# Optimization experiments

Measured on AMD Instinct MI355X. Metric: run time of the kernel, lower is better.

## Reference

```python
import jax, jax.numpy as jnp
import numpy as np

DELTA = 0.1      # delta from __init__
LN_EPS = 1e-5    # torch LayerNorm default eps

B, IN, OUT, E = 256, 512, 512, 256


def setup_inputs() -> dict:
    key = jax.random.key(0)
    ks = jax.random.split(key, 6)
    return {
        "x": jax.random.normal(ks[0], (B, IN), dtype=jnp.float32),
        # nn.init.normal_(std=0.1), shape (out_features, in_features)
        "weights": 0.1 * jax.random.normal(ks[1], (OUT, IN), dtype=jnp.float32),
        # frozen predicate embeddings (in_features, embedding_dim)
        "pred_emb": jax.random.normal(ks[2], (IN, E), dtype=jnp.float32),
        # nn.Linear(E, OUT): weight (OUT, E), bias (OUT,)
        "attn_w": jax.random.uniform(ks[3], (OUT, E), dtype=jnp.float32,
                                      minval=-1.0, maxval=1.0) / np.sqrt(E),
        "attn_b": jax.random.uniform(ks[4], (OUT,), dtype=jnp.float32,
                                      minval=-1.0, maxval=1.0) / np.sqrt(E),
        # nn.LayerNorm(OUT)
        "ln_g": jnp.ones((OUT,), dtype=jnp.float32),
        "ln_b": jnp.zeros((OUT,), dtype=jnp.float32),
    }


def _layernorm(s, g, b):
    mu = s.mean(axis=-1, keepdims=True)
    var = ((s - mu) ** 2).mean(axis=-1, keepdims=True)
    return (s - mu) * jax.lax.rsqrt(var + LN_EPS) * g + b


def reference(x, weights, pred_emb, attn_w, attn_b, ln_g, ln_b):
    # semantic attention gate: batch-invariant, compute once -> (IN, OUT)
    scores = pred_emb @ attn_w.T + attn_b                    # (IN, OUT)
    sig = jax.nn.sigmoid(_layernorm(scores, ln_g, ln_b))     # (IN, OUT)

    xe = x[:, :, None]                                       # (B, IN, 1)
    wt = weights.T[None]                                     # (1, IN, OUT)
    # abs_weight * attn_adjusted, fused elementwise -> (B, IN, OUT)
    aw = jnp.abs(xe * wt) * (sig[None] * xe)

    bias = aw.max(axis=1) - aw.sum(axis=1)                   # CONJUNCTION: max - sum
    return x @ weights.T + DELTA * bias                      # (B, OUT)
```

## Files before the change

### kernel.cpp

```cpp
#include <hip/hip_runtime.h>
#include <hip/hip_bf16.h>
#include <math.h>

#define B_   256
#define IN_  512
#define OUT_ 512
#define E_   256
#define DELTA_ 0.1f
#define LN_EPS_ 1e-5f

__global__ __launch_bounds__(512)
void k1_scores_ln_sig(const float* __restrict__ pred_emb,
                      const float* __restrict__ attn_w,
                      const float* __restrict__ attn_b,
                      const float* __restrict__ ln_g,
                      const float* __restrict__ ln_b,
                      const float* __restrict__ weights,
                      float2* __restrict__ wv) {
    __shared__ float pe[2][E_];
    __shared__ float red[8][2][2];
    __shared__ float smu[2], srs[2];

    const int t    = threadIdx.x;
    const int lane = t & 63;
    const int wid  = t >> 6;
    const int i0   = blockIdx.x * 2;
    const int o    = t;

    pe[t >> 8][t & 255] = pred_emb[(size_t)(i0 + (t >> 8)) * E_ + (t & 255)];
    __syncthreads();

    const float4* p0 = reinterpret_cast<const float4*>(pe[0]);
    const float4* p1 = reinterpret_cast<const float4*>(pe[1]);
    const float4* wrow = reinterpret_cast<const float4*>(attn_w + (size_t)o * E_);

    float a0 = 0.f, a1 = 0.f;
    #pragma unroll 8
    for (int e4 = 0; e4 < E_ / 4; ++e4) {
        float4 w4 = wrow[e4];
        float4 q0 = p0[e4];
        float4 q1 = p1[e4];
        a0 += q0.x * w4.x + q0.y * w4.y + q0.z * w4.z + q0.w * w4.w;
        a1 += q1.x * w4.x + q1.y * w4.y + q1.z * w4.z + q1.w * w4.w;
    }
    const float bo = attn_b[o];
    a0 += bo;
    a1 += bo;

    {
        float s1 = a0, s2 = a0 * a0;
        float u1 = a1, u2 = a1 * a1;
        #pragma unroll
        for (int off = 32; off > 0; off >>= 1) {
            s1 += __shfl_down(s1, off);
            s2 += __shfl_down(s2, off);
            u1 += __shfl_down(u1, off);
            u2 += __shfl_down(u2, off);
        }
        if (lane == 0) {
            red[wid][0][0] = s1; red[wid][0][1] = s2;
            red[wid][1][0] = u1; red[wid][1][1] = u2;
        }
    }
    __syncthreads();
    if (t < 2) {
        float s1 = 0.f, s2 = 0.f;
        #pragma unroll
        for (int w = 0; w < 8; ++w) { s1 += red[w][t][0]; s2 += red[w][t][1]; }
        float mu  = s1 / (float)OUT_;
        float var = s2 / (float)OUT_ - mu * mu;
        smu[t] = mu;
        srs[t] = rsqrtf(var + LN_EPS_);
    }
    __syncthreads();

    const float g  = ln_g[o];
    const float bb = ln_b[o];
    float z0 = (a0 - smu[0]) * srs[0] * g + bb;
    float z1 = (a1 - smu[1]) * srs[1] * g + bb;
    float sg0 = 1.f / (1.f + expf(-z0));
    float sg1 = 1.f / (1.f + expf(-z1));

    float2 w01 = *reinterpret_cast<const float2*>(weights + (size_t)o * IN_ + i0);
    wv[(size_t)(i0 + 0) * OUT_ + o] = make_float2(w01.x, fabsf(w01.x) * sg0);
    wv[(size_t)(i0 + 1) * OUT_ + o] = make_float2(w01.y, fabsf(w01.y) * sg1);
}

#define K2_SK 4
#define K2_CH 128
#define K2_BO (B_ * OUT_)

__global__ __launch_bounds__(256)
void k2_partials(const float* __restrict__ x,
                 const float2* __restrict__ wv,
                 float* __restrict__ plin,
                 float* __restrict__ pmax) {
    __shared__ float4 xs4[64 * 33];
    __shared__ float2 ws2[K2_CH * 17];

    const int t  = threadIdx.x;
    const int ot = t & 15;
    const int bl = t >> 4;
    const int o0 = blockIdx.x * 16;
    const int b0 = blockIdx.y * 64;
    const int sk = blockIdx.z;
    const int i0 = sk * K2_CH;

    #pragma unroll
    for (int k = 0; k < 8; ++k) {
        int p    = t + k * 256;
        int row  = p >> 5;
        int col4 = p & 31;
        xs4[row * 33 + col4] = reinterpret_cast<const float4*>(
            x + (size_t)(b0 + row) * IN_ + i0)[col4];
    }
    #pragma unroll
    for (int k = 0; k < 8; ++k) {
        int r = bl + 16 * k;
        ws2[r * 17 + ot] = wv[(size_t)(i0 + r) * OUT_ + o0 + ot];
    }
    __syncthreads();

    const int o = o0 + ot;
    float d0 = 0.f, s0 = 0.f, m0 = -INFINITY;
    float d1 = 0.f, s1 = 0.f, m1 = -INFINITY;
    float d2 = 0.f, s2 = 0.f, m2 = -INFINITY;
    float d3 = 0.f, s3 = 0.f, m3 = -INFINITY;

    #pragma unroll 2
    for (int i4 = 0; i4 < K2_CH / 4; ++i4) {
        float4 x0 = xs4[(bl +  0) * 33 + i4];
        float4 x1 = xs4[(bl + 16) * 33 + i4];
        float4 x2 = xs4[(bl + 32) * 33 + i4];
        float4 x3 = xs4[(bl + 48) * 33 + i4];
        float2 w0 = ws2[(4 * i4 + 0) * 17 + ot];
        float2 w1 = ws2[(4 * i4 + 1) * 17 + ot];
        float2 w2 = ws2[(4 * i4 + 2) * 17 + ot];
        float2 w3 = ws2[(4 * i4 + 3) * 17 + ot];
        float p;
        float4 u0 = make_float4(x0.x * fabsf(x0.x), x0.y * fabsf(x0.y),
                                x0.z * fabsf(x0.z), x0.w * fabsf(x0.w));
        float4 u1 = make_float4(x1.x * fabsf(x1.x), x1.y * fabsf(x1.y),
                                x1.z * fabsf(x1.z), x1.w * fabsf(x1.w));
        float4 u2 = make_float4(x2.x * fabsf(x2.x), x2.y * fabsf(x2.y),
                                x2.z * fabsf(x2.z), x2.w * fabsf(x2.w));
        float4 u3 = make_float4(x3.x * fabsf(x3.x), x3.y * fabsf(x3.y),
                                x3.z * fabsf(x3.z), x3.w * fabsf(x3.w));

        d0 = fmaf(x0.x, w0.x, d0); p = u0.x * w0.y; s0 += p; m0 = fmaxf(m0, p);
        d1 = fmaf(x1.x, w0.x, d1); p = u1.x * w0.y; s1 += p; m1 = fmaxf(m1, p);
        d2 = fmaf(x2.x, w0.x, d2); p = u2.x * w0.y; s2 += p; m2 = fmaxf(m2, p);
        d3 = fmaf(x3.x, w0.x, d3); p = u3.x * w0.y; s3 += p; m3 = fmaxf(m3, p);

        d0 = fmaf(x0.y, w1.x, d0); p = u0.y * w1.y; s0 += p; m0 = fmaxf(m0, p);
        d1 = fmaf(x1.y, w1.x, d1); p = u1.y * w1.y; s1 += p; m1 = fmaxf(m1, p);
        d2 = fmaf(x2.y, w1.x, d2); p = u2.y * w1.y; s2 += p; m2 = fmaxf(m2, p);
        d3 = fmaf(x3.y, w1.x, d3); p = u3.y * w1.y; s3 += p; m3 = fmaxf(m3, p);

        d0 = fmaf(x0.z, w2.x, d0); p = u0.z * w2.y; s0 += p; m0 = fmaxf(m0, p);
        d1 = fmaf(x1.z, w2.x, d1); p = u1.z * w2.y; s1 += p; m1 = fmaxf(m1, p);
        d2 = fmaf(x2.z, w2.x, d2); p = u2.z * w2.y; s2 += p; m2 = fmaxf(m2, p);
        d3 = fmaf(x3.z, w2.x, d3); p = u3.z * w2.y; s3 += p; m3 = fmaxf(m3, p);

        d0 = fmaf(x0.w, w3.x, d0); p = u0.w * w3.y; s0 += p; m0 = fmaxf(m0, p);
        d1 = fmaf(x1.w, w3.x, d1); p = u1.w * w3.y; s1 += p; m1 = fmaxf(m1, p);
        d2 = fmaf(x2.w, w3.x, d2); p = u2.w * w3.y; s2 += p; m2 = fmaxf(m2, p);
        d3 = fmaf(x3.w, w3.x, d3); p = u3.w * w3.y; s3 += p; m3 = fmaxf(m3, p);
    }

    const size_t base = (size_t)sk * K2_BO + (size_t)b0 * OUT_ + o;
    plin[base + (size_t)(bl +  0) * OUT_] = d0 - DELTA_ * s0;
    plin[base + (size_t)(bl + 16) * OUT_] = d1 - DELTA_ * s1;
    plin[base + (size_t)(bl + 32) * OUT_] = d2 - DELTA_ * s2;
    plin[base + (size_t)(bl + 48) * OUT_] = d3 - DELTA_ * s3;
    pmax[base + (size_t)(bl +  0) * OUT_] = m0;
    pmax[base + (size_t)(bl + 16) * OUT_] = m1;
    pmax[base + (size_t)(bl + 32) * OUT_] = m2;
    pmax[base + (size_t)(bl + 48) * OUT_] = m3;
}

__global__ __launch_bounds__(256)
void k3_combine(const float4* __restrict__ plin4,
                const float4* __restrict__ pmax4,
                float4* __restrict__ out4) {
    const int g = blockIdx.x * 256 + threadIdx.x;
    const int Q = K2_BO / 4;
    float4 l0 = plin4[g], l1 = plin4[Q + g], l2 = plin4[2 * Q + g], l3 = plin4[3 * Q + g];
    float4 m0 = pmax4[g], m1 = pmax4[Q + g], m2 = pmax4[2 * Q + g], m3 = pmax4[3 * Q + g];
    float4 r;
    r.x = (l0.x + l1.x + l2.x + l3.x) + DELTA_ * fmaxf(fmaxf(m0.x, m1.x), fmaxf(m2.x, m3.x));
    r.y = (l0.y + l1.y + l2.y + l3.y) + DELTA_ * fmaxf(fmaxf(m0.y, m1.y), fmaxf(m2.y, m3.y));
    r.z = (l0.z + l1.z + l2.z + l3.z) + DELTA_ * fmaxf(fmaxf(m0.z, m1.z), fmaxf(m2.z, m3.z));
    r.w = (l0.w + l1.w + l2.w + l3.w) + DELTA_ * fmaxf(fmaxf(m0.w, m1.w), fmaxf(m2.w, m3.w));
    out4[g] = r;
}

extern "C" void kernel_launch(void* const* d_in, const int* in_sizes, int n_in,
                              void* d_out, int out_size, void* d_ws, size_t ws_size,
                              hipStream_t stream) {
    const float* x        = (const float*)d_in[0];
    const float* weights  = (const float*)d_in[1];
    const float* pred_emb = (const float*)d_in[2];
    const float* attn_w   = (const float*)d_in[3];
    const float* attn_b   = (const float*)d_in[4];
    const float* ln_g     = (const float*)d_in[5];
    const float* ln_b     = (const float*)d_in[6];

    float2* wv   = (float2*)d_ws;
    float*  plin = (float*)d_ws + 2 * (size_t)IN_ * OUT_;
    float*  pmax = plin + (size_t)K2_SK * K2_BO;

    k1_scores_ln_sig<<<IN_ / 2, 512, 0, stream>>>(
        pred_emb, attn_w, attn_b, ln_g, ln_b, weights, wv);

    k2_partials<<<dim3(OUT_ / 16, B_ / 64, K2_SK), 256, 0, stream>>>(
        x, wv, plin, pmax);

    k3_combine<<<K2_BO / 4 / 256, 256, 0, stream>>>(
        (const float4*)plin, (const float4*)pmax, (float4*)d_out);
}
```

Measured before the change: 99.59 us.

## Remove split-K partials and combine kernel; loop over full IN in one kernel

```diff
diff --git a/kernel.cpp b/kernel.cpp
--- a/kernel.cpp
+++ b/kernel.cpp
@@ -86,113 +86,73 @@
     wv[(size_t)(i0 + 1) * OUT_ + o] = make_float2(w01.y, fabsf(w01.y) * sg1);
 }
 
-#define K2_SK 4
 #define K2_CH 128
-#define K2_BO (B_ * OUT_)
 
 __global__ __launch_bounds__(256)
-void k2_partials(const float* __restrict__ x,
-                 const float2* __restrict__ wv,
-                 float* __restrict__ plin,
-                 float* __restrict__ pmax) {
-    __shared__ float4 xs4[64 * 33];
+void k2_full(const float* __restrict__ x,
+             const float2* __restrict__ wv,
+             float* __restrict__ out) {
+    __shared__ float4 xs4[32 * 33];
     __shared__ float2 ws2[K2_CH * 17];
 
     const int t  = threadIdx.x;
     const int ot = t & 15;
     const int bl = t >> 4;
     const int o0 = blockIdx.x * 16;
-    const int b0 = blockIdx.y * 64;
-    const int sk = blockIdx.z;
-    const int i0 = sk * K2_CH;
+    const int b0 = blockIdx.y * 32;
+    const int o  = o0 + ot;
 
-    #pragma unroll
-    for (int k = 0; k < 8; ++k) {
-        int p    = t + k * 256;
-        int row  = p >> 5;
-        int col4 = p & 31;
-        xs4[row * 33 + col4] = reinterpret_cast<const float4*>(
-            x + (size_t)(b0 + row) * IN_ + i0)[col4];
-    }
-    #pragma unroll
-    for (int k = 0; k < 8; ++k) {
-        int r = bl + 16 * k;
-        ws2[r * 17 + ot] = wv[(size_t)(i0 + r) * OUT_ + o0 + ot];
-    }
-    __syncthreads();
-
-    const int o = o0 + ot;
     float d0 = 0.f, s0 = 0.f, m0 = -INFINITY;
     float d1 = 0.f, s1 = 0.f, m1 = -INFINITY;
-    float d2 = 0.f, s2 = 0.f, m2 = -INFINITY;
-    float d3 = 0.f, s3 = 0.f, m3 = -INFINITY;
 
-    #pragma unroll 2
-    for (int i4 = 0; i4 < K2_CH / 4; ++i4) {
-        float4 x0 = xs4[(bl +  0) * 33 + i4];
-        float4 x1 = xs4[(bl + 16) * 33 + i4];
-        float4 x2 = xs4[(bl + 32) * 33 + i4];
-        float4 x3 = xs4[(bl + 48) * 33 + i4];
-        float2 w0 = ws2[(4 * i4 + 0) * 17 + ot];
-        float2 w1 = ws2[(4 * i4 + 1) * 17 + ot];
-        float2 w2 = ws2[(4 * i4 + 2) * 17 + ot];
-        float2 w3 = ws2[(4 * i4 + 3) * 17 + ot];
-        float p;
-        float4 u0 = make_float4(x0.x * fabsf(x0.x), x0.y * fabsf(x0.y),
-                                x0.z * fabsf(x0.z), x0.w * fabsf(x0.w));
-        float4 u1 = make_float4(x1.x * fabsf(x1.x), x1.y * fabsf(x1.y),
-                                x1.z * fabsf(x1.z), x1.w * fabsf(x1.w));
-        float4 u2 = make_float4(x2.x * fabsf(x2.x), x2.y * fabsf(x2.y),
-                                x2.z * fabsf(x2.z), x2.w * fabsf(x2.w));
-        float4 u3 = make_float4(x3.x * fabsf(x3.x), x3.y * fabsf(x3.y),
-                                x3.z * fabsf(x3.z), x3.w * fabsf(x3.w));
+    for (int c = 0; c < IN_ / K2_CH; ++c) {
+        if (c) __syncthreads();
+        const int i0 = c * K2_CH;
 
-        d0 = fmaf(x0.x, w0.x, d0); p = u0.x * w0.y; s0 += p; m0 = fmaxf(m0, p);
-        d1 = fmaf(x1.x, w0.x, d1); p = u1.x * w0.y; s1 += p; m1 = fmaxf(m1, p);
-        d2 = fmaf(x2.x, w0.x, d2); p = u2.x * w0.y; s2 += p; m2 = fmaxf(m2, p);
-        d3 = fmaf(x3.x, w0.x, d3); p = u3.x * w0.y; s3 += p; m3 = fmaxf(m3, p);
+        #pragma unroll
+        for (int k = 0; k < 4; ++k) {
+            int p    = t + k * 256;
+            int row  = p >> 5;
+            int col4 = p & 31;
+            xs4[row * 33 + col4] = reinterpret_cast<const float4*>(
+                x + (size_t)(b0 + row) * IN_ + i0)[col4];
+        }
+        #pragma unroll
+        for (int k = 0; k < 8; ++k) {
+            int r = bl + 16 * k;
+            ws2[r * 17 + ot] = wv[(size_t)(i0 + r) * OUT_ + o0 + ot];
+        }
+        __syncthreads();
 
-        d0 = fmaf(x0.y, w1.x, d0); p = u0.y * w1.y; s0 += p; m0 = fmaxf(m0, p);
-        d1 = fmaf(x1.y, w1.x, d1); p = u1.y * w1.y; s1 += p; m1 = fmaxf(m1, p);
-        d2 = fmaf(x2.y, w1.x, d2); p = u2.y * w1.y; s2 += p; m2 = fmaxf(m2, p);
-        d3 = fmaf(x3.y, w1.x, d3); p = u3.y * w1.y; s3 += p; m3 = fmaxf(m3, p);
-
-        d0 = fmaf(x0.z, w2.x, d0); p = u0.z * w2.y; s0 += p; m0 = fmaxf(m0, p);
-        d1 = fmaf(x1.z, w2.x, d1); p = u1.z * w2.y; s1 += p; m1 = fmaxf(m1, p);
-        d2 = fmaf(x2.z, w2.x, d2); p = u2.z * w2.y; s2 += p; m2 = fmaxf(m2, p);
-        d3 = fmaf(x3.z, w2.x, d3); p = u3.z * w2.y; s3 += p; m3 = fmaxf(m3, p);
-
-        d0 = fmaf(x0.w, w3.x, d0); p = u0.w * w3.y; s0 += p; m0 = fmaxf(m0, p);
-        d1 = fmaf(x1.w, w3.x, d1); p = u1.w * w3.y; s1 += p; m1 = fmaxf(m1, p);
-        d2 = fmaf(x2.w, w3.x, d2); p = u2.w * w3.y; s2 += p; m2 = fmaxf(m2, p);
-        d3 = fmaf(x3.w, w3.x, d3); p = u3.w * w3.y; s3 += p; m3 = fmaxf(m3, p);
+        #pragma unroll 4
+        for (int i4 = 0; i4 < K2_CH / 4; ++i4) {
+            float4 xa = xs4[(bl +  0) * 33 + i4];
+            float4 xb = xs4[(bl + 16) * 33 + i4];
+            float2 w0 = ws2[(4 * i4 + 0) * 17 + ot];
+            float2 w1 = ws2[(4 * i4 + 1) * 17 + ot];
+            float2 w2 = ws2[(4 * i4 + 2) * 17 + ot];
+            float2 w3 = ws2[(4 * i4 + 3) * 17 + ot];
+            float4 ua = make_float4(xa.x * fabsf(xa.x), xa.y * fabsf(xa.y),
+                                    xa.z * fabsf(xa.z), xa.w * fabsf(xa.w));
+            float4 ub = make_float4(xb.x * fabsf(xb.x), xb.y * fabsf(xb.y),
+                                    xb.z * fabsf(xb.z), xb.w * fabsf(xb.w));
+            float pa0 = ua.x * w0.y, pa1 = ua.y * w1.y,
+                  pa2 = ua.z * w2.y, pa3 = ua.w * w3.y;
+            float pb0 = ub.x * w0.y, pb1 = ub.y * w1.y,
+                  pb2 = ub.z * w2.y, pb3 = ub.w * w3.y;
+            d0 = fmaf(xa.x, w0.x, d0); d0 = fmaf(xa.y, w1.x, d0);
+            d0 = fmaf(xa.z, w2.x, d0); d0 = fmaf(xa.w, w3.x, d0);
+            d1 = fmaf(xb.x, w0.x, d1); d1 = fmaf(xb.y, w1.x, d1);
+            d1 = fmaf(xb.z, w2.x, d1); d1 = fmaf(xb.w, w3.x, d1);
+            s0 += pa0 + pa1 + pa2 + pa3;
+            s1 += pb0 + pb1 + pb2 + pb3;
+            m0 = fmaxf(m0, fmaxf(fmaxf(pa0, pa1), fmaxf(pa2, pa3)));
+            m1 = fmaxf(m1, fmaxf(fmaxf(pb0, pb1), fmaxf(pb2, pb3)));
+        }
     }
 
-    const size_t base = (size_t)sk * K2_BO + (size_t)b0 * OUT_ + o;
-    plin[base + (size_t)(bl +  0) * OUT_] = d0 - DELTA_ * s0;
-    plin[base + (size_t)(bl + 16) * OUT_] = d1 - DELTA_ * s1;
-    plin[base + (size_t)(bl + 32) * OUT_] = d2 - DELTA_ * s2;
-    plin[base + (size_t)(bl + 48) * OUT_] = d3 - DELTA_ * s3;
-    pmax[base + (size_t)(bl +  0) * OUT_] = m0;
-    pmax[base + (size_t)(bl + 16) * OUT_] = m1;
-    pmax[base + (size_t)(bl + 32) * OUT_] = m2;
-    pmax[base + (size_t)(bl + 48) * OUT_] = m3;
-}
-
-__global__ __launch_bounds__(256)
-void k3_combine(const float4* __restrict__ plin4,
-                const float4* __restrict__ pmax4,
-                float4* __restrict__ out4) {
-    const int g = blockIdx.x * 256 + threadIdx.x;
-    const int Q = K2_BO / 4;
-    float4 l0 = plin4[g], l1 = plin4[Q + g], l2 = plin4[2 * Q + g], l3 = plin4[3 * Q + g];
-    float4 m0 = pmax4[g], m1 = pmax4[Q + g], m2 = pmax4[2 * Q + g], m3 = pmax4[3 * Q + g];
-    float4 r;
-    r.x = (l0.x + l1.x + l2.x + l3.x) + DELTA_ * fmaxf(fmaxf(m0.x, m1.x), fmaxf(m2.x, m3.x));
-    r.y = (l0.y + l1.y + l2.y + l3.y) + DELTA_ * fmaxf(fmaxf(m0.y, m1.y), fmaxf(m2.y, m3.y));
-    r.z = (l0.z + l1.z + l2.z + l3.z) + DELTA_ * fmaxf(fmaxf(m0.z, m1.z), fmaxf(m2.z, m3.z));
-    r.w = (l0.w + l1.w + l2.w + l3.w) + DELTA_ * fmaxf(fmaxf(m0.w, m1.w), fmaxf(m2.w, m3.w));
-    out4[g] = r;
+    out[(size_t)(b0 + bl +  0) * OUT_ + o] = d0 + DELTA_ * (m0 - s0);
+    out[(size_t)(b0 + bl + 16) * OUT_ + o] = d1 + DELTA_ * (m1 - s1);
 }
 
 extern "C" void kernel_launch(void* const* d_in, const int* in_sizes, int n_in,
@@ -206,16 +166,10 @@
     const float* ln_g     = (const float*)d_in[5];
     const float* ln_b     = (const float*)d_in[6];
 
-    float2* wv   = (float2*)d_ws;
-    float*  plin = (float*)d_ws + 2 * (size_t)IN_ * OUT_;
-    float*  pmax = plin + (size_t)K2_SK * K2_BO;
+    float2* wv = (float2*)d_ws;
 
     k1_scores_ln_sig<<<IN_ / 2, 512, 0, stream>>>(
         pred_emb, attn_w, attn_b, ln_g, ln_b, weights, wv);
 
-    k2_partials<<<dim3(OUT_ / 16, B_ / 64, K2_SK), 256, 0, stream>>>(
-        x, wv, plin, pmax);
-
-    k3_combine<<<K2_BO / 4 / 256, 256, 0, stream>>>(
-        (const float4*)plin, (const float4*)pmax, (float4*)d_out);
+    k2_full<<<dim3(OUT_ / 16, B_ / 32), 256, 0, stream>>>(x, wv, (float*)d_out);
 }
```

Measured after the change: 103.0 us. 1.03x slower.
